# Performance work log

Measured on AMD Instinct MI355X. Metric: run time of the kernel, lower is better.

## Reference

```python
import jax, jax.numpy as jnp
import numpy as np
import math

BLANK_THRESHOLD = 0.95  # __init__ blank_threshlod


def setup_inputs() -> dict:
    key = jax.random.key(0)
    k1, k2, k3, k4, k5 = jax.random.split(key, 5)
    N, T, C, V = 16, 2048, 512, 1024
    x = jax.random.normal(k1, (N, T, C), dtype=jnp.float32)
    # ctc_output holds log-posteriors; only the blank column is read.
    # Make blank posterior realistic: mostly high (blank-dominant frames),
    ctc_output = jax.random.normal(k2, (N, T, V), dtype=jnp.float32)
    blank_post = jax.random.uniform(k5, (N, T), minval=0.90, maxval=1.0)
    ctc_output = ctc_output.at[:, :, 0].set(jnp.log(blank_post))
    x_lens = jax.random.randint(k3, (N,), T // 2, T + 1)
    y_lens = jax.random.randint(k4, (N,), 64, 512)
    return {"x": x, "x_lens": x_lens, "ctc_output": ctc_output,
            "y_lens": y_lens, "blank_id": 0}


def reference(x, x_lens, ctc_output, y_lens, blank_id):
    N, T, C = x.shape
    t_idx = jnp.arange(T)
    # padding positions are True
    padding_mask = t_idx[None, :] >= x_lens[:, None]          # [N, T]
    blank_lp = ctc_output[:, :, blank_id]                     # [N, T]
    non_blank_mask = (blank_lp < math.log(BLANK_THRESHOLD)) & (~padding_mask)
    # y_lens branch: topk over blank posteriors selects, per row n, the
    # top-(T - y_lens[n]) most-blank frames (the torch remainder/gather/scatter
    # construction is exactly this set). Frames NOT in that set are force-kept.
    limit_lens = T - y_lens                                   # [N]
    # rank 0 = largest blank log-posterior (equivalent to topk membership)
    ranks = jnp.argsort(jnp.argsort(-blank_lp, axis=1), axis=1)
    limit_mask = ranks < limit_lens[:, None]                  # [N, T]
    non_blank_mask = non_blank_mask | (~limit_mask)
    out_lens = non_blank_mask.sum(axis=1)                     # [N]
    # stream compaction: stable-sort kept frames to the front of each row
    order = jnp.argsort(~non_blank_mask, axis=1, stable=True) # [N, T]
    out = jnp.take_along_axis(x, order[:, :, None], axis=1)   # [N, T, C]
    # zero the tail (torch pads with zeros); output padded to static T
    valid = t_idx[None, :] < out_lens[:, None]
    out = out * valid[:, :, None].astype(x.dtype)
    return out, out_lens
```

## Files before the change

### kernel.cpp

```cpp
#include <hip/hip_runtime.h>
#include <math.h>

#define TT 2048
#define CC 512
#define VV 1024

__global__ __launch_bounds__(256) void flags_kernel(
    const float* __restrict__ ctc, const int* __restrict__ x_lens,
    const int* __restrict__ y_lens, const int* __restrict__ blank_id,
    int* __restrict__ flags) {
  const int n = blockIdx.y;
  const int chunk = blockIdx.x;
  __shared__ float sv[TT];
  const int bid = blank_id[0];
  const float* row = ctc + (size_t)n * TT * VV + bid;
  for (int i = threadIdx.x; i < TT; i += 256) sv[i] = row[(size_t)i * VV];
  __syncthreads();

  const int t = chunk * 256 + threadIdx.x;
  const float vt = sv[t];
  int cnt = 0;
#pragma unroll 8
  for (int s = 0; s < TT; ++s) {
    float w = sv[s];
    cnt += (w > vt || (w == vt && s < t)) ? 1 : 0;
  }
  const int limit = TT - y_lens[n];
  const float LOG_T = (float)-0.05129329438755058;
  const int keep = ((vt < LOG_T) && (t < x_lens[n])) || (cnt >= limit);
  flags[n * TT + t] = keep;
}

__global__ __launch_bounds__(256) void scan_kernel(
    const int* __restrict__ flags, int* __restrict__ src_map,
    int* __restrict__ out_lens_i, float* __restrict__ out_lens_f) {
  const int n = blockIdx.x;
  const int tid = threadIdx.x;
  int f[8];
  const int base = n * TT + tid * 8;
  int local = 0;
#pragma unroll
  for (int k = 0; k < 8; ++k) {
    f[k] = flags[base + k];
    local += f[k];
  }
  __shared__ int ssum[256];
  ssum[tid] = local;
  __syncthreads();
  for (int off = 1; off < 256; off <<= 1) {
    int v = (tid >= off) ? ssum[tid - off] : 0;
    __syncthreads();
    ssum[tid] += v;
    __syncthreads();
  }
  int pos = ssum[tid] - local;
  const int total = ssum[255];
#pragma unroll
  for (int k = 0; k < 8; ++k) {
    if (f[k]) {
      src_map[n * TT + pos] = tid * 8 + k;
      ++pos;
    }
  }
  if (tid == 0) {
    out_lens_i[n] = total;
    out_lens_f[n] = (float)total;
  }
}

__global__ __launch_bounds__(256) void gather_kernel(
    const float4* __restrict__ x, const int* __restrict__ src_map,
    const int* __restrict__ out_lens_i, float4* __restrict__ out) {
  const size_t idx = (size_t)blockIdx.x * 256 + threadIdx.x;
  const int c4 = (int)(idx & 127);
  const size_t row = idx >> 7;
  const int j = (int)(row & (TT - 1));
  const int n = (int)(row >> 11);
  float4 val;
  if (j < out_lens_i[n]) {
    const int src = src_map[n * TT + j];
    val = x[(((size_t)n * TT + src) << 7) + c4];
  } else {
    val = make_float4(0.f, 0.f, 0.f, 0.f);
  }
  out[idx] = val;
}

extern "C" void kernel_launch(void* const* d_in, const int* in_sizes, int n_in,
                              void* d_out, int out_size, void* d_ws, size_t ws_size,
                              hipStream_t stream) {
  const float* x = (const float*)d_in[0];
  const int* x_lens = (const int*)d_in[1];
  const float* ctc = (const float*)d_in[2];
  const int* y_lens = (const int*)d_in[3];
  const int* blank_id = (const int*)d_in[4];
  float* out = (float*)d_out;
  const int N = in_sizes[1];

  int* flags = (int*)d_ws;
  int* src_map = flags + N * TT;
  int* out_lens_i = src_map + N * TT;
  float* out_lens_f = out + (size_t)N * TT * CC;

  flags_kernel<<<dim3(TT / 256, N), 256, 0, stream>>>(ctc, x_lens, y_lens,
                                                      blank_id, flags);
  scan_kernel<<<N, 256, 0, stream>>>(flags, src_map, out_lens_i, out_lens_f);

  const int total4 = N * TT * (CC / 4);
  gather_kernel<<<total4 / 256, 256, 0, stream>>>((const float4*)x, src_map,
                                                  out_lens_i, (float4*)out);
}
```

Before: 278.2 us.

## Replace O(T^2) rank counting with radix select and fuse scan into one kernel

Drops the all-pairs rank counting, where each frame compared itself against all T blank values. In its place, a 4-pass 8-bit radix select finds the K-th order threshold key over order-preserving float keys, with ties broken by index through a prefix scan. Keep flags and the compaction scan are computed in the same kernel, which removes the flags buffer and one launch. Only N blocks of 256 threads now run the selection, so parallelism is low and each pass relies on shared-memory atomics and block-wide syncs.

```diff
diff --git a/kernel.cpp b/kernel.cpp
--- a/kernel.cpp
+++ b/kernel.cpp
@@ -1,70 +1,120 @@
 #include <hip/hip_runtime.h>
-#include <math.h>
 
 #define TT 2048
 #define CC 512
 #define VV 1024
+#define NTHR 256
+#define EPT 8
 
-__global__ __launch_bounds__(256) void flags_kernel(
+__device__ __forceinline__ unsigned int fkey(float f) {
+  unsigned int b = __float_as_uint(f);
+  return b ^ ((b & 0x80000000u) ? 0xFFFFFFFFu : 0x80000000u);
+}
+
+__device__ __forceinline__ int block_scan_incl(int v, int* wsum, int tid) {
+#pragma unroll
+  for (int off = 1; off < 64; off <<= 1) {
+    int u = __shfl_up(v, off, 64);
+    if ((tid & 63) >= off) v += u;
+  }
+  const int wave = tid >> 6;
+  if ((tid & 63) == 63) wsum[wave] = v;
+  __syncthreads();
+  int add = 0;
+#pragma unroll
+  for (int w = 0; w < 3; ++w) add += (w < wave) ? wsum[w] : 0;
+  v += add;
+  __syncthreads();
+  return v;
+}
+
+__global__ __launch_bounds__(256) void select_scan_kernel(
     const float* __restrict__ ctc, const int* __restrict__ x_lens,
     const int* __restrict__ y_lens, const int* __restrict__ blank_id,
-    int* __restrict__ flags) {
-  const int n = blockIdx.y;
-  const int chunk = blockIdx.x;
-  __shared__ float sv[TT];
+    int* __restrict__ src_map, int* __restrict__ out_lens_i,
+    float* __restrict__ out_lens_f) {
+  const int n = blockIdx.x;
+  const int tid = threadIdx.x;
+  __shared__ int hist[256];
+  __shared__ int wsum[4];
+  __shared__ int bsel[3];
+  __shared__ int stotal;
+
   const int bid = blank_id[0];
   const float* row = ctc + (size_t)n * TT * VV + bid;
-  for (int i = threadIdx.x; i < TT; i += 256) sv[i] = row[(size_t)i * VV];
+  unsigned int myk[EPT];
+#pragma unroll
+  for (int k = 0; k < EPT; ++k) {
+    const int t = tid * EPT + k;
+    myk[k] = fkey(row[(size_t)t * VV]);
+  }
+
+  int Kp = y_lens[n];
+  unsigned int prefix = 0;
+  int M = 0;
+#pragma unroll
+  for (int r = 3; r >= 0; --r) {
+    hist[tid] = 0;
+    __syncthreads();
+    const int sh = r * 8;
+#pragma unroll
+    for (int k = 0; k < EPT; ++k) {
+      const unsigned int u = myk[k];
+      const bool act =
+          (r == 3) || (((unsigned long long)u >> (sh + 8)) ==
+                       ((unsigned long long)prefix >> (sh + 8)));
+      if (act) atomicAdd(&hist[(u >> sh) & 0xFF], 1);
+    }
+    __syncthreads();
+    const int own = hist[tid];
+    const int cum = block_scan_incl(own, wsum, tid);
+    const int excl = cum - own;
+    if (own > 0 && excl < Kp && cum >= Kp) {
+      bsel[0] = tid;
+      bsel[1] = Kp - excl;
+      bsel[2] = own;
+    }
+    __syncthreads();
+    prefix |= ((unsigned int)bsel[0]) << sh;
+    Kp = bsel[1];
+    if (r == 0) M = bsel[2];
+  }
+  const unsigned int theta = prefix;
+
+  int eqc = 0;
+#pragma unroll
+  for (int k = 0; k < EPT; ++k) eqc += (myk[k] == theta) ? 1 : 0;
+  const int eq_incl = block_scan_incl(eqc, wsum, tid);
+  int e = eq_incl - eqc;
+
+  const unsigned int KEY_THR = fkey((float)-0.05129329438755058);
+  const int xl = x_lens[n];
+  int keepf[EPT];
+  int kc = 0;
+#pragma unroll
+  for (int k = 0; k < EPT; ++k) {
+    const int t = tid * EPT + k;
+    const unsigned int u = myk[k];
+    const bool eq = (u == theta);
+    const bool forced = (u < theta) || (eq && (e >= M - Kp));
+    const bool keep = ((u < KEY_THR) && (t < xl)) || forced;
+    if (eq) ++e;
+    keepf[k] = keep ? 1 : 0;
+    kc += keepf[k];
+  }
+
+  const int k_incl = block_scan_incl(kc, wsum, tid);
+  int pos = k_incl - kc;
+  if (tid == NTHR - 1) stotal = k_incl;
+  int* smrow = src_map + n * TT;
+#pragma unroll
+  for (int k = 0; k < EPT; ++k) {
+    if (keepf[k]) smrow[pos++] = tid * EPT + k;
+  }
   __syncthreads();
-
-  const int t = chunk * 256 + threadIdx.x;
-  const float vt = sv[t];
-  int cnt = 0;
-#pragma unroll 8
-  for (int s = 0; s < TT; ++s) {
-    float w = sv[s];
-    cnt += (w > vt || (w == vt && s < t)) ? 1 : 0;
-  }
-  const int limit = TT - y_lens[n];
-  const float LOG_T = (float)-0.05129329438755058;
-  const int keep = ((vt < LOG_T) && (t < x_lens[n])) || (cnt >= limit);
-  flags[n * TT + t] = keep;
-}
-
-__global__ __launch_bounds__(256) void scan_kernel(
-    const int* __restrict__ flags, int* __restrict__ src_map,
-    int* __restrict__ out_lens_i, float* __restrict__ out_lens_f) {
-  const int n = blockIdx.x;
-  const int tid = threadIdx.x;
-  int f[8];
-  const int base = n * TT + tid * 8;
-  int local = 0;
-#pragma unroll
-  for (int k = 0; k < 8; ++k) {
-    f[k] = flags[base + k];
-    local += f[k];
-  }
-  __shared__ int ssum[256];
-  ssum[tid] = local;
-  __syncthreads();
-  for (int off = 1; off < 256; off <<= 1) {
-    int v = (tid >= off) ? ssum[tid - off] : 0;
-    __syncthreads();
-    ssum[tid] += v;
-    __syncthreads();
-  }
-  int pos = ssum[tid] - local;
-  const int total = ssum[255];
-#pragma unroll
-  for (int k = 0; k < 8; ++k) {
-    if (f[k]) {
-      src_map[n * TT + pos] = tid * 8 + k;
-      ++pos;
-    }
-  }
   if (tid == 0) {
-    out_lens_i[n] = total;
-    out_lens_f[n] = (float)total;
+    out_lens_i[n] = stotal;
+    out_lens_f[n] = (float)stotal;
   }
 }
 
@@ -97,14 +147,12 @@
   float* out = (float*)d_out;
   const int N = in_sizes[1];
 
-  int* flags = (int*)d_ws;
-  int* src_map = flags + N * TT;
+  int* src_map = (int*)d_ws;
   int* out_lens_i = src_map + N * TT;
   float* out_lens_f = out + (size_t)N * TT * CC;
 
-  flags_kernel<<<dim3(TT / 256, N), 256, 0, stream>>>(ctc, x_lens, y_lens,
-                                                      blank_id, flags);
-  scan_kernel<<<N, 256, 0, stream>>>(flags, src_map, out_lens_i, out_lens_f);
+  select_scan_kernel<<<N, NTHR, 0, stream>>>(ctc, x_lens, y_lens, blank_id,
+                                             src_map, out_lens_i, out_lens_f);
 
   const int total4 = N * TT * (CC / 4);
   gather_kernel<<<total4 / 256, 256, 0, stream>>>((const float4*)x, src_map,
```

Measured after the change: 229.2 us (median of 2 runs). 1.21x faster.
